# Kernel optimization log

Measured on AMD Instinct MI355X. Metric: run time of the kernel, lower is better.

Reference implementation:

```python
import jax, jax.numpy as jnp
import numpy as np

Z, N, Ki, Dm, H = 2, 2048, 32, 256, 4
Dk = Dm // H


def _film(x, cond, W1, b1, W2, b2):
    # MLP(d_in=Dm, d_hidden=Dm, d_out=2*Dm, 1 hidden layer, silu)
    h = jax.nn.silu(cond @ W1 + b1)
    gb = h @ W2 + b2
    gamma, beta = jnp.split(gb, 2, axis=-1)
    return gamma * x + beta


def setup_inputs() -> dict:
    key = jax.random.key(0)
    ks = jax.random.split(key, 16)
    xav = (6.0 / (Dk + Dm)) ** 0.5
    mlp_s = (1.0 / Dm) ** 0.5
    inp = {
        "nodes_i": jax.random.normal(ks[0], (Z, N, Dm), jnp.float32),
        "edges": jax.random.normal(ks[1], (Z, N, Ki, Dm), jnp.float32),
        "nodes_j": jax.random.normal(ks[2], (Z, N, Ki, Dm), jnp.float32),
        "nbr_mask": jax.random.bernoulli(ks[3], 0.5, (Z, N, Ki)),
        # FiLM K mlp
        "fk_W1": jax.random.uniform(ks[4], (Dm, Dm), jnp.float32, -mlp_s, mlp_s),
        "fk_b1": jnp.zeros((Dm,), jnp.float32),
        "fk_W2": jax.random.uniform(ks[5], (Dm, 2 * Dm), jnp.float32, -mlp_s, mlp_s),
        "fk_b2": jnp.zeros((2 * Dm,), jnp.float32),
        # FiLM V mlp
        "fv_W1": jax.random.uniform(ks[6], (Dm, Dm), jnp.float32, -mlp_s, mlp_s),
        "fv_b1": jnp.zeros((Dm,), jnp.float32),
        "fv_W2": jax.random.uniform(ks[7], (Dm, 2 * Dm), jnp.float32, -mlp_s, mlp_s),
        "fv_b2": jnp.zeros((2 * Dm,), jnp.float32),
        # attention projections
        "q_proj": jax.random.uniform(ks[8], (H, Dm, Dk), jnp.float32, -xav, xav),
        "k_proj": jax.random.uniform(ks[9], (H, Dm, Dk), jnp.float32, -xav, xav),
        "v_proj": jax.random.uniform(ks[10], (H, Dm, Dk), jnp.float32, -xav, xav),
        "q_bias": jnp.zeros((H, Dk), jnp.float32),
        "k_bias": jnp.zeros((H, Dk), jnp.float32),
        "v_bias": jnp.zeros((H, Dk), jnp.float32),
        "out_W": jax.random.uniform(ks[11], (Dm, Dm), jnp.float32, -mlp_s, mlp_s),
    }
    return inp


def reference(nodes_i, edges, nodes_j, nbr_mask,
              fk_W1, fk_b1, fk_W2, fk_b2,
              fv_W1, fv_b1, fv_W2, fv_b2,
              q_proj, k_proj, v_proj, q_bias, k_bias, v_bias, out_W):
    z, n, ki, dm = nodes_j.shape
    # FiLM edge conditioning of neighbor features
    k_in = _film(nodes_j, edges, fk_W1, fk_b1, fk_W2, fk_b2)  # [Z,N,Ki,Dm]
    v_in = _film(nodes_j, edges, fv_W1, fv_b1, fv_W2, fv_b2)  # [Z,N,Ki,Dm]
    # multi-head projections
    Q = jnp.einsum('znd,hde->zhne', nodes_i, q_proj) + q_bias[None, :, None, :]
    K = jnp.einsum('znkd,hde->zhnke', k_in, k_proj) + k_bias[None, :, None, None, :]
    V = jnp.einsum('znkd,hde->zhnke', v_in, v_proj) + v_bias[None, :, None, None, :]
    # scores over neighbor dim Ki
    S = jnp.einsum('zhne,zhnke->zhnk', Q, K) / (Q.shape[-1] ** 0.5)
    # mask: -inf for non-neighbors, unless the whole row is masked (then no mask)
    inv = ~nbr_mask  # [Z,N,Ki]
    attn_mask = inv & ~jnp.all(inv, axis=-1, keepdims=True)
    S = jnp.where(attn_mask[:, None, :, :], -jnp.inf, S)
    P = jax.nn.softmax(S, axis=-1)
    out = jnp.einsum('zhnk,zhnke->zhne', P, V)  # [Z,H,N,Dk]
    # torch: permute(0,2,3,1).reshape(Z,N,Dm) -> flatten order (Dk, H)
    out = jnp.transpose(out, (0, 2, 3, 1)).reshape(z, n, dm)
    # nn.Linear(bias=False): y = x @ W.T
    return out @ out_W.T
```

## Files before the change

kernel.cpp:

```cpp
#include <hip/hip_runtime.h>
#include <stdint.h>

#define NNODE 2048
#define KI 32
#define DM 256

using short8 = __attribute__((ext_vector_type(8))) short;
using f32x4  = __attribute__((ext_vector_type(4))) float;

#define WU_OFF   1024
#define BIAS_OFF 1312768

__device__ __forceinline__ float bf2f(uint16_t u){
  union { uint32_t i; float f; } v; v.i = ((uint32_t)u) << 16; return v.f;
}
__device__ __forceinline__ uint16_t f2bf(float f){
  union { float f; uint32_t i; } v; v.f = f;
  uint32_t x = v.i;
  return (uint16_t)((x + 0x7FFFu + ((x >> 16) & 1u)) >> 16);
}
__device__ __forceinline__ float read_f(const void* p, long idx, int fbf){
  return fbf ? bf2f(((const uint16_t*)p)[idx]) : ((const float*)p)[idx];
}

__global__ void sniff_kernel(const uint32_t* ni, const uint32_t* mask, int* flags){
  __shared__ int cnt[6];
  int t = threadIdx.x;
  if (t < 6) cnt[t] = 0;
  __syncthreads();
  {
    uint32_t u = ni[t];
    uint32_t lo = u & 0xFFFFu;
    uint32_t exl = (lo >> 7) & 0xFFu;
    if ((lo & 0x7FFFu) == 0u || (exl >= 100u && exl <= 140u)) atomicAdd(&cnt[0], 1);
  }
  if (t < 64){
    uint32_t u = mask[t];
    if (!(u == 0u || u == 1u)) atomicAdd(&cnt[1], 1);
    if (!(u == 0u || u == 0x3F800000u)) atomicAdd(&cnt[2], 1);
    uint32_t lo = u & 0xFFFFu, hi = u >> 16;
    if (!((lo == 0u || lo == 0x3F80u) && (hi == 0u || hi == 0x3F80u))) atomicAdd(&cnt[3], 1);
    if ((t & 1) && u != 0u) atomicAdd(&cnt[4], 1);
    if (!(t & 1) && u == 1u) atomicAdd(&cnt[5], 1);
  }
  __syncthreads();
  if (t == 0){
    flags[0] = (cnt[0] >= 160) ? 1 : 0;
    int mk;
    if (cnt[1] == 0) mk = (cnt[4] == 0 && cnt[5] > 0) ? 4 : 0;
    else if (cnt[2] == 0) mk = 3;
    else if (cnt[3] == 0) mk = 2;
    else mk = 1;
    flags[1] = mk;
  }
}

__global__ void prep_kernel(const void* fkW1, const void* fkb1, const void* fkW2, const void* fkb2,
                            const void* fvW1, const void* fvb1, const void* fvW2, const void* fvb2,
                            const void* qW, const void* kW, const void* vW,
                            const void* qb, const void* kb, const void* vb,
                            const void* oW, void* wsv){
  char* ws = (char*)wsv;
  const int fbf = ((const int*)ws)[0];
  uint16_t* wu = (uint16_t*)(ws + WU_OFF);
  float* bias = (float*)(ws + BIAS_OFF);
  const int total = 655360 + 2304;
  for (int o = blockIdx.x*blockDim.x + threadIdx.x; o < total; o += gridDim.x*blockDim.x){
    if (o < 655360){
      const void* src; long si;
      if (o < 131072){
        int t = o & 65535;
        src = (o < 65536) ? fkW1 : fvW1;
        int j = t & 7, l = (t >> 3) & 63, ks = (t >> 9) & 7, nt = t >> 12;
        int n = nt*16 + (l & 15);
        int k = ks*32 + ((l >> 4) << 3) + j;
        si = (long)k*256 + n;
      } else if (o < 393216){
        int oo = o - 131072;
        int t = oo & 131071;
        src = (oo < 131072) ? fkW2 : fvW2;
        int j = t & 7, l = (t >> 3) & 63, ks = (t >> 9) & 7, nt = t >> 12;
        int n = nt*16 + (l & 15);
        int k = ks*32 + ((l >> 4) << 3) + j;
        si = (long)k*512 + n;
      } else if (o < 524288){
        int oo = o - 393216;
        int t = oo & 65535;
        src = (oo < 65536) ? kW : vW;
        int j = t & 7, l = (t >> 3) & 63, ks = (t >> 9) & 7, nt = t >> 12;
        int n = nt*16 + (l & 15);
        int k = ks*32 + ((l >> 4) << 3) + j;
        si = (long)(n >> 6)*16384 + (long)k*64 + (n & 63);
      } else if (o < 589824){
        int t = o - 524288;
        int col = t >> 8, d = t & 255;
        src = qW;
        si = (long)(col >> 6)*16384 + (long)d*64 + (col & 63);
      } else {
        int t = o - 589824;
        src = oW;
        si = t;
      }
      wu[o] = f2bf(read_f(src, si, fbf));
    } else {
      int bo = o - 655360;
      const void* src; long si;
      if (bo < 256){ src = fkb1; si = bo; }
      else if (bo < 768){ src = fkb2; si = bo - 256; }
      else if (bo < 1024){ src = fvb1; si = bo - 768; }
      else if (bo < 1536){ src = fvb2; si = bo - 1024; }
      else if (bo < 1792){ src = kb; si = bo - 1536; }
      else if (bo < 2048){ src = vb; si = bo - 1792; }
      else { src = qb; si = bo - 2048; }
      bias[bo] = read_f(src, si, fbf);
    }
  }
}

__device__ __forceinline__ int swz_off(int row, int col){
  return row*256 + ((col & 248) ^ ((row & 7) << 3)) + (col & 7);
}
__device__ __forceinline__ short8 lda(const uint16_t* buf, int mt, int ks, int lane){
  int row = mt*16 + (lane & 15);
  int kc  = ks*4 + (lane >> 4);
  int off = row*256 + (((kc << 3) ^ ((row & 7) << 3)));
  return *(const short8*)(buf + off);
}
__device__ __forceinline__ short8 ldb(const uint16_t* W, int nt, int ks, int lane){
  return *(const short8*)(W + ((((nt << 3) + ks) << 6) + lane) * 8);
}
__device__ __forceinline__ f32x4 mfma16(short8 a, short8 b, f32x4 c){
  return __builtin_amdgcn_mfma_f32_16x16x32_bf16(a, b, c, 0, 0, 0);
}

__device__ __forceinline__ void gemm1_kv(const uint16_t* src,
                                         const uint16_t* W1k, const float* b1k, uint16_t* dstK,
                                         const uint16_t* W1v, const float* b1v, uint16_t* dstV,
                                         int lane, int nh){
  const int cl = lane & 15, kg = lane >> 4;
  f32x4 ak[2][4], av[2][4];
  #pragma unroll
  for (int i = 0; i < 4; i++){
    float bk = b1k[(nh*4 + i)*16 + cl];
    float bv = b1v[(nh*4 + i)*16 + cl];
    f32x4 ck = {bk,bk,bk,bk}, cv = {bv,bv,bv,bv};
    ak[0][i] = ck; ak[1][i] = ck;
    av[0][i] = cv; av[1][i] = cv;
  }
  #pragma unroll
  for (int ks = 0; ks < 8; ks++){
    short8 a0 = lda(src, 0, ks, lane);
    short8 a1 = lda(src, 1, ks, lane);
    #pragma unroll
    for (int i = 0; i < 4; i++){
      short8 bk = ldb(W1k, nh*4 + i, ks, lane);
      short8 bv = ldb(W1v, nh*4 + i, ks, lane);
      ak[0][i] = mfma16(a0, bk, ak[0][i]);
      ak[1][i] = mfma16(a1, bk, ak[1][i]);
      av[0][i] = mfma16(a0, bv, av[0][i]);
      av[1][i] = mfma16(a1, bv, av[1][i]);
    }
  }
  #pragma unroll
  for (int m = 0; m < 2; m++){
    int rowb = m*16 + kg*4;
    #pragma unroll
    for (int i = 0; i < 4; i++){
      int col = (nh*4 + i)*16 + cl;
      #pragma unroll
      for (int r = 0; r < 4; r++){
        float vk = ak[m][i][r];
        float vv = av[m][i][r];
        dstK[swz_off(rowb + r, col)] = f2bf(vk / (1.0f + __expf(-vk)));
        dstV[swz_off(rowb + r, col)] = f2bf(vv / (1.0f + __expf(-vv)));
      }
    }
  }
}

__device__ __forceinline__ void gemm2_film(const uint16_t* src, const uint16_t* W2, const float* b2,
                                           const uint16_t* xj, uint16_t* dst, int lane, int nh){
  const int cl = lane & 15, kg = lane >> 4;
  #pragma unroll
  for (int ch = 0; ch < 2; ch++){
    f32x4 ag[2][2], ab[2][2];
    #pragma unroll
    for (int j = 0; j < 2; j++){
      int dt = nh*4 + ch*2 + j;
      float bg = b2[dt*16 + cl];
      float bb = b2[(16 + dt)*16 + cl];
      f32x4 cg = {bg,bg,bg,bg}, cb = {bb,bb,bb,bb};
      ag[0][j] = cg; ag[1][j] = cg; ab[0][j] = cb; ab[1][j] = cb;
    }
    #pragma unroll
    for (int ks = 0; ks < 8; ks++){
      short8 a0 = lda(src, 0, ks, lane);
      short8 a1 = lda(src, 1, ks, lane);
      #pragma unroll
      for (int j = 0; j < 2; j++){
        int dt = nh*4 + ch*2 + j;
        short8 bg = ldb(W2, dt, ks, lane);
        short8 bb = ldb(W2, 16 + dt, ks, lane);
        ag[0][j] = mfma16(a0, bg, ag[0][j]);
        ag[1][j] = mfma16(a1, bg, ag[1][j]);
        ab[0][j] = mfma16(a0, bb, ab[0][j]);
        ab[1][j] = mfma16(a1, bb, ab[1][j]);
      }
    }
    #pragma unroll
    for (int m = 0; m < 2; m++){
      int rowb = m*16 + kg*4;
      #pragma unroll
      for (int j = 0; j < 2; j++){
        int d = (nh*4 + ch*2 + j)*16 + cl;
        #pragma unroll
        for (int r = 0; r < 4; r++){
          int row = rowb + r;
          float x = bf2f(xj[swz_off(row, d)]);
          dst[swz_off(row, d)] = f2bf(ag[m][j][r] * x + ab[m][j][r]);
        }
      }
    }
  }
}

__device__ __forceinline__ void gemm3_scores(const uint16_t* src, const uint16_t* W, const float* bs,
                                             const float* sQ, float (*sS)[4], int lane, int nh){
  const int cl = lane & 15, kg = lane >> 4;
  f32x4 acc[2][4];
  #pragma unroll
  for (int i = 0; i < 4; i++){
    float bb = bs[(nh*4 + i)*16 + cl];
    f32x4 c = {bb,bb,bb,bb};
    acc[0][i] = c; acc[1][i] = c;
  }
  #pragma unroll
  for (int ks = 0; ks < 8; ks++){
    short8 a0 = lda(src, 0, ks, lane);
    short8 a1 = lda(src, 1, ks, lane);
    #pragma unroll
    for (int i = 0; i < 4; i++){
      short8 bv = ldb(W, nh*4 + i, ks, lane);
      acc[0][i] = mfma16(a0, bv, acc[0][i]);
      acc[1][i] = mfma16(a1, bv, acc[1][i]);
    }
  }
  #pragma unroll
  for (int m = 0; m < 2; m++){
    int rowb = m*16 + kg*4;
    float p0=0.f, p1=0.f, p2=0.f, p3=0.f;
    #pragma unroll
    for (int i = 0; i < 4; i++){
      float qv = sQ[(nh*4 + i)*16 + cl];
      p0 += acc[m][i][0]*qv; p1 += acc[m][i][1]*qv;
      p2 += acc[m][i][2]*qv; p3 += acc[m][i][3]*qv;
    }
    float pr[4] = {p0, p1, p2, p3};
    #pragma unroll
    for (int r = 0; r < 4; r++){
      float v = pr[r];
      v += __shfl_xor(v, 1, 16);
      v += __shfl_xor(v, 2, 16);
      v += __shfl_xor(v, 4, 16);
      v += __shfl_xor(v, 8, 16);
      if (cl == 0) sS[rowb + r][nh] = v;
    }
  }
}

__device__ __forceinline__ void gemm3_store(const uint16_t* src, const uint16_t* W, const float* bs,
                                            uint16_t* dst, int lane, int nh){
  const int cl = lane & 15, kg = lane >> 4;
  f32x4 acc[2][4];
  #pragma unroll
  for (int i = 0; i < 4; i++){
    float bb = bs[(nh*4 + i)*16 + cl];
    f32x4 c = {bb,bb,bb,bb};
    acc[0][i] = c; acc[1][i] = c;
  }
  #pragma unroll
  for (int ks = 0; ks < 8; ks++){
    short8 a0 = lda(src, 0, ks, lane);
    short8 a1 = lda(src, 1, ks, lane);
    #pragma unroll
    for (int i = 0; i < 4; i++){
      short8 bv = ldb(W, nh*4 + i, ks, lane);
      acc[0][i] = mfma16(a0, bv, acc[0][i]);
      acc[1][i] = mfma16(a1, bv, acc[1][i]);
    }
  }
  #pragma unroll
  for (int m = 0; m < 2; m++){
    int rowb = m*16 + kg*4;
    #pragma unroll
    for (int i = 0; i < 4; i++){
      int col = (nh*4 + i)*16 + cl;
      #pragma unroll
      for (int r = 0; r < 4; r++)
        dst[swz_off(rowb + r, col)] = f2bf(acc[m][i][r]);
    }
  }
}

__launch_bounds__(256, 1)
__global__ void fused_kernel(const void* nodes_i, const void* edges, const void* nodes_j, const void* maskp,
                             const void* wsv, float* out)
{
  const char* ws = (const char*)wsv;
  const int* flags = (const int*)ws;
  const int fbf = flags[0], mk = flags[1];
  const uint16_t* wu = (const uint16_t*)(ws + WU_OFF);
  const float* bias = (const float*)(ws + BIAS_OFF);
  const uint16_t* W1k = wu;
  const uint16_t* W1v = wu + 65536;
  const uint16_t* W2k = wu + 131072;
  const uint16_t* W2v = wu + 262144;
  const uint16_t* KBw = wu + 393216;
  const uint16_t* VBw = wu + 458752;
  const uint16_t* QBt = wu + 524288;
  const uint16_t* WoB = wu + 589824;
  const float* b1k = bias;
  const float* b2k = bias + 256;
  const float* b1v = bias + 768;
  const float* b2v = bias + 1024;
  const float* kbb = bias + 1536;
  const float* vbb = bias + 1792;
  const float* qbb = bias + 2048;

  __shared__ __align__(16) uint16_t bufE[KI*DM];
  __shared__ __align__(16) uint16_t bufXJ[KI*DM];
  __shared__ __align__(16) uint16_t bufA[KI*DM];
  __shared__ __align__(16) uint16_t bufB[KI*DM];
  __shared__ float sQ[DM];
  __shared__ float sNI[DM];
  __shared__ float sS[KI][4];
  __shared__ float sP[KI][4];
  __shared__ float sO[DM];

  const int tid = threadIdx.x;
  const int lane = tid & 63;
  const int nh = tid >> 6;
  const int b = blockIdx.x;
  const int z = b >> 11;
  const int n = b & 2047;
  const long ebase = ((long)(z*NNODE + n)) * (KI*DM);
  const long nbase = ((long)(z*NNODE + n)) * DM;

  sNI[tid] = read_f(nodes_i, nbase + tid, fbf);
  if (fbf){
    const uint16_t* xp = (const uint16_t*)nodes_j;
    const uint16_t* ep = (const uint16_t*)edges;
    for (int c = tid; c < 2048; c += 256){
      int sel = c >> 10, cc = c & 1023;
      int row = cc >> 5, kc = cc & 31;
      const uint16_t* src = sel ? ep : xp;
      uint16_t* dst = sel ? bufE : bufXJ;
      short8 v = *(const short8*)(src + ebase + row*256 + kc*8);
      *(short8*)(dst + row*256 + (((kc << 3) ^ ((row & 7) << 3)))) = v;
    }
  } else {
    const float* xp = (const float*)nodes_j;
    const float* ep = (const float*)edges;
    for (int c = tid; c < 2048; c += 256){
      int sel = c >> 10, cc = c & 1023;
      int row = cc >> 5, kc = cc & 31;
      const float* src = (sel ? ep : xp) + ebase + row*256 + kc*8;
      uint16_t* dst = sel ? bufE : bufXJ;
      f32x4 x0 = *(const f32x4*)src;
      f32x4 x1 = *(const f32x4*)(src + 4);
      short8 v;
      v[0]=(short)f2bf(x0[0]); v[1]=(short)f2bf(x0[1]); v[2]=(short)f2bf(x0[2]); v[3]=(short)f2bf(x0[3]);
      v[4]=(short)f2bf(x1[0]); v[5]=(short)f2bf(x1[1]); v[6]=(short)f2bf(x1[2]); v[7]=(short)f2bf(x1[3]);
      *(short8*)(dst + row*256 + (((kc << 3) ^ ((row & 7) << 3)))) = v;
    }
  }
  __syncthreads();

  {
    const uint16_t* wrow = QBt + tid*256;
    float a = qbb[tid];
    for (int d = 0; d < 256; d += 8){
      short8 wv = *(const short8*)(wrow + d);
      #pragma unroll
      for (int j = 0; j < 8; j++)
        a += sNI[d + j] * bf2f((uint16_t)wv[j]);
    }
    sQ[tid] = a * 0.125f;
  }
  gemm1_kv(bufE, W1k, b1k, bufA, W1v, b1v, bufB, lane, nh);
  __syncthreads();

  gemm2_film(bufA, W2k, b2k, bufXJ, bufE, lane, nh);
  __syncthreads();

  gemm3_scores(bufE, KBw, kbb, sQ, sS, lane, nh);
  gemm2_film(bufB, W2v, b2v, bufXJ, bufA, lane, nh);
  __syncthreads();

  gemm3_store(bufA, VBw, vbb, bufB, lane, nh);
  if (tid < 128){
    int h2 = tid >> 5, k2 = tid & 31;
    long mi = (long)(z*NNODE + n)*KI + k2;
    bool mval;
    if (mk == 0)      mval = ((const int*)maskp)[mi] != 0;
    else if (mk == 1) mval = ((const unsigned char*)maskp)[mi] != 0;
    else if (mk == 2) mval = ((const uint16_t*)maskp)[mi] != 0;
    else if (mk == 4) mval = ((const int*)maskp)[mi*2] != 0;
    else              mval = ((const float*)maskp)[mi] != 0.0f;
    unsigned long long bal = __ballot(mval);
    unsigned int gm = (unsigned int)(bal >> (tid & 32));
    bool anyT = (gm != 0u);
    float s = sS[k2][h2];
    if (anyT && !mval) s = -1e30f;
    float mx = s;
    mx = fmaxf(mx, __shfl_xor(mx, 16, 32));
    mx = fmaxf(mx, __shfl_xor(mx,  8, 32));
    mx = fmaxf(mx, __shfl_xor(mx,  4, 32));
    mx = fmaxf(mx, __shfl_xor(mx,  2, 32));
    mx = fmaxf(mx, __shfl_xor(mx,  1, 32));
    float e = __expf(s - mx);
    float su = e;
    su += __shfl_xor(su, 16, 32);
    su += __shfl_xor(su,  8, 32);
    su += __shfl_xor(su,  4, 32);
    su += __shfl_xor(su,  2, 32);
    su += __shfl_xor(su,  1, 32);
    sP[k2][h2] = e / su;
  }
  __syncthreads();

  {
    int h = tid >> 6;
    float a = 0.0f;
    #pragma unroll 4
    for (int k = 0; k < KI; k++)
      a += sP[k][h] * bf2f(bufB[swz_off(k, tid)]);
    sO[(tid & 63)*4 + h] = a;
  }
  __syncthreads();

  {
    const uint16_t* wrow = WoB + tid*256;
    float a = 0.0f;
    for (int m8 = 0; m8 < 256; m8 += 8){
      short8 wv = *(const short8*)(wrow + m8);
      #pragma unroll
      for (int j = 0; j < 8; j++)
        a += sO[m8 + j] * bf2f((uint16_t)wv[j]);
    }
    out[nbase + tid] = a;
  }
}

extern "C" void kernel_launch(void* const* d_in, const int* in_sizes, int n_in,
                              void* d_out, int out_size, void* d_ws, size_t ws_size,
                              hipStream_t stream){
  int* flags = (int*)d_ws;
  sniff_kernel<<<1, 256, 0, stream>>>((const uint32_t*)d_in[0], (const uint32_t*)d_in[3], flags);
  prep_kernel<<<1024, 256, 0, stream>>>(d_in[4], d_in[5], d_in[6], d_in[7],
                                        d_in[8], d_in[9], d_in[10], d_in[11],
                                        d_in[12], d_in[13], d_in[14],
                                        d_in[15], d_in[16], d_in[17],
                                        d_in[18], d_ws);
  fused_kernel<<<2*NNODE, 256, 0, stream>>>(d_in[0], d_in[1], d_in[2], d_in[3], d_ws, (float*)d_out);
}
```

Before: 570.1 us.

## Process two nodes per 512-thread block with duplicated shared buffers

Each block now runs 512 threads as two independent 256-thread groups, each handling its own node with its own copy of the LDS buffers. The grid is halved. The change also inserts a scheduling barrier between the score GEMM and the V FiLM GEMM. The aim is to share weight fetches through cache between the two groups and to let one group's work overlap the other's stalls. In exchange LDS use per block doubles and the block-wide syncs now couple both groups, which may lower occupancy.

```diff
diff --git a/kernel.cpp b/kernel.cpp
--- a/kernel.cpp
+++ b/kernel.cpp
@@ -302,7 +302,7 @@
   }
 }
 
-__launch_bounds__(256, 1)
+__launch_bounds__(512, 1)
 __global__ void fused_kernel(const void* nodes_i, const void* edges, const void* nodes_j, const void* maskp,
                              const void* wsv, float* out)
 {
@@ -327,45 +327,47 @@
   const float* vbb = bias + 1792;
   const float* qbb = bias + 2048;
 
-  __shared__ __align__(16) uint16_t bufE[KI*DM];
-  __shared__ __align__(16) uint16_t bufXJ[KI*DM];
-  __shared__ __align__(16) uint16_t bufA[KI*DM];
-  __shared__ __align__(16) uint16_t bufB[KI*DM];
-  __shared__ float sQ[DM];
-  __shared__ float sNI[DM];
-  __shared__ float sS[KI][4];
-  __shared__ float sP[KI][4];
-  __shared__ float sO[DM];
+  __shared__ __align__(16) uint16_t bufE[2][KI*DM];
+  __shared__ __align__(16) uint16_t bufXJ[2][KI*DM];
+  __shared__ __align__(16) uint16_t bufA[2][KI*DM];
+  __shared__ __align__(16) uint16_t bufB[2][KI*DM];
+  __shared__ float sQ[2][DM];
+  __shared__ float sNI[2][DM];
+  __shared__ float sS[2][KI][4];
+  __shared__ float sP[2][KI][4];
+  __shared__ float sO[2][DM];
 
   const int tid = threadIdx.x;
+  const int g = tid >> 8;
+  const int th = tid & 255;
   const int lane = tid & 63;
-  const int nh = tid >> 6;
+  const int nh = (tid >> 6) & 3;
   const int b = blockIdx.x;
-  const int z = b >> 11;
-  const int n = b & 2047;
+  const int z = b >> 10;
+  const int n = (b & 1023)*2 + g;
   const long ebase = ((long)(z*NNODE + n)) * (KI*DM);
   const long nbase = ((long)(z*NNODE + n)) * DM;
 
-  sNI[tid] = read_f(nodes_i, nbase + tid, fbf);
+  sNI[g][th] = read_f(nodes_i, nbase + th, fbf);
   if (fbf){
     const uint16_t* xp = (const uint16_t*)nodes_j;
     const uint16_t* ep = (const uint16_t*)edges;
-    for (int c = tid; c < 2048; c += 256){
+    for (int c = th; c < 2048; c += 256){
       int sel = c >> 10, cc = c & 1023;
       int row = cc >> 5, kc = cc & 31;
       const uint16_t* src = sel ? ep : xp;
-      uint16_t* dst = sel ? bufE : bufXJ;
+      uint16_t* dst = sel ? bufE[g] : bufXJ[g];
       short8 v = *(const short8*)(src + ebase + row*256 + kc*8);
       *(short8*)(dst + row*256 + (((kc << 3) ^ ((row & 7) << 3)))) = v;
     }
   } else {
     const float* xp = (const float*)nodes_j;
     const float* ep = (const float*)edges;
-    for (int c = tid; c < 2048; c += 256){
+    for (int c = th; c < 2048; c += 256){
       int sel = c >> 10, cc = c & 1023;
       int row = cc >> 5, kc = cc & 31;
       const float* src = (sel ? ep : xp) + ebase + row*256 + kc*8;
-      uint16_t* dst = sel ? bufE : bufXJ;
+      uint16_t* dst = sel ? bufE[g] : bufXJ[g];
       f32x4 x0 = *(const f32x4*)src;
       f32x4 x1 = *(const f32x4*)(src + 4);
       short8 v;
@@ -377,29 +379,30 @@
   __syncthreads();
 
   {
-    const uint16_t* wrow = QBt + tid*256;
-    float a = qbb[tid];
+    const uint16_t* wrow = QBt + th*256;
+    float a = qbb[th];
     for (int d = 0; d < 256; d += 8){
       short8 wv = *(const short8*)(wrow + d);
       #pragma unroll
       for (int j = 0; j < 8; j++)
-        a += sNI[d + j] * bf2f((uint16_t)wv[j]);
-    }
-    sQ[tid] = a * 0.125f;
-  }
-  gemm1_kv(bufE, W1k, b1k, bufA, W1v, b1v, bufB, lane, nh);
-  __syncthreads();
-
-  gemm2_film(bufA, W2k, b2k, bufXJ, bufE, lane, nh);
-  __syncthreads();
-
-  gemm3_scores(bufE, KBw, kbb, sQ, sS, lane, nh);
-  gemm2_film(bufB, W2v, b2v, bufXJ, bufA, lane, nh);
-  __syncthreads();
-
-  gemm3_store(bufA, VBw, vbb, bufB, lane, nh);
-  if (tid < 128){
-    int h2 = tid >> 5, k2 = tid & 31;
+        a += sNI[g][d + j] * bf2f((uint16_t)wv[j]);
+    }
+    sQ[g][th] = a * 0.125f;
+  }
+  gemm1_kv(bufE[g], W1k, b1k, bufA[g], W1v, b1v, bufB[g], lane, nh);
+  __syncthreads();
+
+  gemm2_film(bufA[g], W2k, b2k, bufXJ[g], bufE[g], lane, nh);
+  __syncthreads();
+
+  gemm3_scores(bufE[g], KBw, kbb, sQ[g], sS[g], lane, nh);
+  __builtin_amdgcn_sched_barrier(0);
+  gemm2_film(bufB[g], W2v, b2v, bufXJ[g], bufA[g], lane, nh);
+  __syncthreads();
+
+  gemm3_store(bufA[g], VBw, vbb, bufB[g], lane, nh);
+  if (th < 128){
+    int h2 = th >> 5, k2 = th & 31;
     long mi = (long)(z*NNODE + n)*KI + k2;
     bool mval;
     if (mk == 0)      mval = ((const int*)maskp)[mi] != 0;
@@ -410,7 +413,7 @@
     unsigned long long bal = __ballot(mval);
     unsigned int gm = (unsigned int)(bal >> (tid & 32));
     bool anyT = (gm != 0u);
-    float s = sS[k2][h2];
+    float s = sS[g][k2][h2];
     if (anyT && !mval) s = -1e30f;
     float mx = s;
     mx = fmaxf(mx, __shfl_xor(mx, 16, 32));
@@ -425,30 +428,30 @@
     su += __shfl_xor(su,  4, 32);
     su += __shfl_xor(su,  2, 32);
     su += __shfl_xor(su,  1, 32);
-    sP[k2][h2] = e / su;
+    sP[g][k2][h2] = e / su;
   }
   __syncthreads();
 
   {
-    int h = tid >> 6;
+    int h = th >> 6;
     float a = 0.0f;
     #pragma unroll 4
     for (int k = 0; k < KI; k++)
-      a += sP[k][h] * bf2f(bufB[swz_off(k, tid)]);
-    sO[(tid & 63)*4 + h] = a;
+      a += sP[g][k][h] * bf2f(bufB[g][swz_off(k, th)]);
+    sO[g][(th & 63)*4 + h] = a;
   }
   __syncthreads();
 
   {
-    const uint16_t* wrow = WoB + tid*256;
+    const uint16_t* wrow = WoB + th*256;
     float a = 0.0f;
     for (int m8 = 0; m8 < 256; m8 += 8){
       short8 wv = *(const short8*)(wrow + m8);
       #pragma unroll
       for (int j = 0; j < 8; j++)
-        a += sO[m8 + j] * bf2f((uint16_t)wv[j]);
-    }
-    out[nbase + tid] = a;
+        a += sO[g][m8 + j] * bf2f((uint16_t)wv[j]);
+    }
+    out[nbase + th] = a;
   }
 }
 
@@ -462,5 +465,5 @@
                                         d_in[12], d_in[13], d_in[14],
                                         d_in[15], d_in[16], d_in[17],
                                         d_in[18], d_ws);
-  fused_kernel<<<2*NNODE, 256, 0, stream>>>(d_in[0], d_in[1], d_in[2], d_in[3], d_ws, (float*)d_out);
-}
+  fused_kernel<<<NNODE, 512, 0, stream>>>(d_in[0], d_in[1], d_in[2], d_in[3], d_ws, (float*)d_out);
+}
```

New measurement: 635.8 us. 1.12x slower.
